# Kernel optimization log

Hardware: AMD Instinct MI355X
Metric: run time of the kernel (lower is better)

The kernel has to match this reference:

```python
import jax, jax.numpy as jnp
import numpy as np

FEAT_DIM = 4
TOKEN_DIM = 256
HIDDEN = [256, 256]
B, N, T = 512, 512, 4
BN_EPS = 1e-5


def setup_inputs() -> dict:
    key = jax.random.key(0)
    ks = jax.random.split(key, 10)
    bbox_ltwh = jax.random.uniform(ks[0], (B, N, T, FEAT_DIM), dtype=jnp.float32)
    mask = jax.random.randint(ks[1], (B, N), 0, 2).astype(bool)
    # MLP params: Linear(4->256)+BN+ReLU, Linear(256->256)+BN+ReLU, Linear(256->256)
    def lin(k, fan_in, fan_out):
        bound = 1.0 / np.sqrt(fan_in)
        kw, kb = jax.random.split(k)
        W = jax.random.uniform(kw, (fan_in, fan_out), minval=-bound, maxval=bound, dtype=jnp.float32)
        b = jax.random.uniform(kb, (fan_out,), minval=-bound, maxval=bound, dtype=jnp.float32)
        return W, b
    W1, b1 = lin(ks[2], FEAT_DIM, HIDDEN[0])
    W2, b2 = lin(ks[3], HIDDEN[0], HIDDEN[1])
    W3, b3 = lin(ks[4], HIDDEN[1], TOKEN_DIM)
    g1 = jnp.ones((HIDDEN[0],), jnp.float32); be1 = jnp.zeros((HIDDEN[0],), jnp.float32)
    g2 = jnp.ones((HIDDEN[1],), jnp.float32); be2 = jnp.zeros((HIDDEN[1],), jnp.float32)
    return {"bbox_ltwh": bbox_ltwh, "mask": mask,
            "W1": W1, "b1": b1, "g1": g1, "be1": be1,
            "W2": W2, "b2": b2, "g2": g2, "be2": be2,
            "W3": W3, "b3": b3}


def _masked_bn(h, m, cnt, gamma, beta):
    # BatchNorm1d (training mode) over only the valid (masked-in) rows.
    mu = jnp.sum(h * m, axis=0) / cnt
    var = jnp.sum(jnp.square(h - mu) * m, axis=0) / cnt
    return (h - mu) * jax.lax.rsqrt(var + BN_EPS) * gamma + beta


def reference(bbox_ltwh, mask, W1, b1, g1, be1, W2, b2, g2, be2, W3, b3):
    # last bbox of each tracklet: [B, N, 4] -> [B*N, 4]
    x = bbox_ltwh[:, :, 0].reshape(-1, FEAT_DIM)
    m = mask.reshape(-1).astype(x.dtype)[:, None]  # [B*N, 1]
    cnt = jnp.maximum(jnp.sum(m), 1.0)
    # Equivalent to gather(valid) -> MLP -> scatter into zeros: compute on all
    # rows with BN statistics taken over valid rows only, then zero invalid rows.
    h = jax.nn.relu(_masked_bn(x @ W1 + b1, m, cnt, g1, be1))
    h = jax.nn.relu(_masked_bn(h @ W2 + b2, m, cnt, g2, be2))
    h = h @ W3 + b3
    out = (h * m).reshape(B, N, TOKEN_DIM)
    return out
```

## Files before the change

### kernel.cpp

```cpp
#include <hip/hip_runtime.h>

typedef __attribute__((ext_vector_type(8))) short short8;
typedef __attribute__((ext_vector_type(4))) float f32x4;

#define M_ROWS (512*512)
#define NTILES (M_ROWS/64)
#define GRID_SETUP 512
#define GRID_STATS 512
#define GRID_MLP 256
#define ROWS_MLP (M_ROWS/GRID_MLP)
#define TILES_MLP (ROWS_MLP/64)
#define BN_EPS_F 1e-5f

#define WS_P1   64
#define WS_CNT  12352
#define WS_A1   12416
#define WS_D1   13440
#define WS_A2   13696
#define WS_C2   13952
#define WS_W2T  14336
#define WS_W3T  47104
#define WS_P2   79872

__device__ __forceinline__ float load_mask(const void* mp, int fmt, int row) {
  return fmt ? (((const unsigned char*)mp)[row] ? 1.f : 0.f)
             : (((const int*)mp)[row] ? 1.f : 0.f);
}

__device__ __forceinline__ ushort f2bf(float f) {
  unsigned int u = __float_as_uint(f);
  u += 0x7FFFu + ((u >> 16) & 1u);
  return (ushort)(u >> 16);
}

__device__ __forceinline__ void barrier_lds() {
  __builtin_amdgcn_sched_barrier(0);
  asm volatile("s_waitcnt lgkmcnt(0)");
  __builtin_amdgcn_sched_barrier(0);
  __builtin_amdgcn_s_barrier();
  __builtin_amdgcn_sched_barrier(0);
}

__device__ __forceinline__ void compute_h1(
    const float (*xs)[4], ushort* h1s, int t,
    const float a1c[4][2], const float d1c[2]) {
  const int c0 = (t & 127) * 2;
  const int r0 = (t >> 7) * 32;
  #pragma unroll 4
  for (int rr = 0; rr < 32; ++rr) {
    const int r = r0 + rr;
    const f32x4 xv = *(const f32x4*)&xs[r][0];
    float v0 = d1c[0], v1 = d1c[1];
    v0 = fmaf(xv.x, a1c[0][0], v0); v1 = fmaf(xv.x, a1c[0][1], v1);
    v0 = fmaf(xv.y, a1c[1][0], v0); v1 = fmaf(xv.y, a1c[1][1], v1);
    v0 = fmaf(xv.z, a1c[2][0], v0); v1 = fmaf(xv.z, a1c[2][1], v1);
    v0 = fmaf(xv.w, a1c[3][0], v0); v1 = fmaf(xv.w, a1c[3][1], v1);
    v0 = fmaxf(v0, 0.f); v1 = fmaxf(v1, 0.f);
    unsigned int pk = (unsigned int)f2bf(v0) | ((unsigned int)f2bf(v1) << 16);
    unsigned int byte = (unsigned int)r*512u + (unsigned int)c0*2u;
    byte ^= (unsigned int)(r & 7) << 4;
    *(unsigned int*)((char*)h1s + byte) = pk;
  }
}

__device__ __forceinline__ void load_aF(const ushort* h1s, int lane, int ks,
                                        int kb, short8 aF[4]) {
  #pragma unroll
  for (int rf = 0; rf < 4; ++rf) {
    const int row = rf*16 + (lane & 15);
    unsigned int byte = (unsigned int)row*512u + (unsigned int)((ks*32 + kb)*2);
    byte ^= (unsigned int)(row & 7) << 4;
    aF[rf] = *(const short8*)((const char*)h1s + byte);
  }
}

__device__ __forceinline__ void gemm_reg(const ushort* h1s,
    const short8 Br[4][8], int lane, f32x4 acc[4][4]) {
  const int kb = (lane >> 4) * 8;
  #pragma unroll
  for (int ks = 0; ks < 8; ++ks) {
    short8 aF[4];
    load_aF(h1s, lane, ks, kb, aF);
    #pragma unroll
    for (int cf = 0; cf < 4; ++cf)
      #pragma unroll
      for (int rf = 0; rf < 4; ++rf)
        acc[rf][cf] = __builtin_amdgcn_mfma_f32_16x16x32_bf16(
            aF[rf], Br[cf][ks], acc[rf][cf], 0, 0, 0);
  }
}

__device__ __forceinline__ void load_B(const ushort* __restrict__ Wt,
                                       int lane, int wave, short8 Br[4][8]) {
  const int kb = (lane >> 4) * 8;
  const ushort* wp = Wt + (size_t)(wave*64 + (lane & 15))*256 + kb;
  #pragma unroll
  for (int cf = 0; cf < 4; ++cf)
    #pragma unroll
    for (int ks = 0; ks < 8; ++ks)
      Br[cf][ks] = *(const short8*)(wp + cf*4096 + ks*32);
}

__global__ __launch_bounds__(256) void setup_kernel(
    const float* __restrict__ bbox, const void* __restrict__ maskp,
    const float* __restrict__ W2, const float* __restrict__ W3,
    float* __restrict__ wsf) {
  __shared__ int s_fmt;
  __shared__ float red[256][22];
  const int t = threadIdx.x, b = blockIdx.x;
  if (t == 0) s_fmt = 0;
  __syncthreads();
  {
    const uint4 v = ((const uint4*)maskp)[t];
    if (((v.x | v.y | v.z | v.w) & 0xFFFFFF00u) != 0u) s_fmt = 1;
  }
  __syncthreads();
  const int fmt = s_fmt;

  float own[21];
  #pragma unroll
  for (int i = 0; i < 21; ++i) own[i] = 0.f;
  #pragma unroll
  for (int i = 0; i < 2; ++i) {
    const int row = b*512 + i*256 + t;
    const float m = load_mask(maskp, fmt, row);
    if (m != 0.f) {
      float4 x4 = *(const float4*)(bbox + (size_t)row * 16);
      float xv[4] = {x4.x, x4.y, x4.z, x4.w};
      own[0] += 1.f;
      #pragma unroll
      for (int i2 = 0; i2 < 4; ++i2) {
        own[1+i2] += xv[i2];
        #pragma unroll
        for (int j = 0; j < 4; ++j)
          own[5+i2*4+j] = fmaf(xv[i2], xv[j], own[5+i2*4+j]);
      }
    }
  }
  #pragma unroll
  for (int s = 0; s < 21; ++s) red[t][s] = own[s];
  __syncthreads();
  for (int off = 128; off > 0; off >>= 1) {
    if (t < off) {
      #pragma unroll
      for (int s = 0; s < 21; ++s) red[t][s] += red[t+off][s];
    }
    __syncthreads();
  }
  if (t < 21) wsf[WS_P1 + b*24 + t] = red[0][t];

  if (b < 256) {
    ((ushort*)(wsf + WS_W2T))[t*256 + b] = f2bf(W2[b*256 + t]);
  } else {
    const int bb = b - 256;
    ((ushort*)(wsf + WS_W3T))[t*256 + bb] = f2bf(W3[bb*256 + t]);
  }
}

__global__ __launch_bounds__(256) void finalize1_kernel(
    const float* __restrict__ part, const float* __restrict__ W1,
    const float* __restrict__ b1, const float* __restrict__ g1,
    const float* __restrict__ be1, float* __restrict__ wsf) {
  __shared__ float red[256][22];
  __shared__ float sarr[21];
  const int t = threadIdx.x;
  #pragma unroll
  for (int s = 0; s < 21; ++s)
    red[t][s] = part[t*24 + s] + part[(t+256)*24 + s];
  __syncthreads();
  for (int off = 128; off > 0; off >>= 1) {
    if (t < off) {
      #pragma unroll
      for (int s = 0; s < 21; ++s) red[t][s] += red[t+off][s];
    }
    __syncthreads();
  }
  if (t < 21) sarr[t] = red[0][t];
  __syncthreads();
  float s[21];
  #pragma unroll
  for (int i = 0; i < 21; ++i) s[i] = sarr[i];
  const float cnt = fmaxf(s[0], 1.f);
  float w[4] = {W1[t], W1[256+t], W1[512+t], W1[768+t]};
  const float b1f = b1[t];
  float sw = 0.f;
  #pragma unroll
  for (int k = 0; k < 4; ++k) sw = fmaf(s[1+k], w[k], sw);
  float qf = 0.f;
  #pragma unroll
  for (int i = 0; i < 4; ++i)
    #pragma unroll
    for (int j = 0; j < 4; ++j) qf = fmaf(s[5+i*4+j]*w[i], w[j], qf);
  const float mu  = sw/cnt + b1f;
  const float eh2 = (qf + 2.f*b1f*sw)/cnt + b1f*b1f;
  const float var = fmaxf(eh2 - mu*mu, 0.f);
  const float a1  = g1[t] * rsqrtf(var + BN_EPS_F);
  const float c1  = be1[t] - mu*a1;
  #pragma unroll
  for (int k = 0; k < 4; ++k) wsf[WS_A1 + k*256 + t] = w[k]*a1;
  wsf[WS_D1 + t] = fmaf(b1f, a1, c1);
  if (t == 0) wsf[WS_CNT] = cnt;
}

__global__ __launch_bounds__(256, 2) void stats2_mfma(
    const float* __restrict__ bbox, const void* __restrict__ maskp,
    const float* wsf, const float* __restrict__ b2,
    float* __restrict__ part2) {
  __shared__ float xs[64][4];
  __shared__ float ms[64];
  __shared__ ushort h1s[64*256];
  __shared__ int s_fmt;
  const int t = threadIdx.x, lane = t & 63, wave = t >> 6;
  if (t == 0) s_fmt = 0;
  __syncthreads();
  {
    const uint4 v = ((const uint4*)maskp)[t];
    if (((v.x | v.y | v.z | v.w) & 0xFFFFFF00u) != 0u) s_fmt = 1;
  }
  __syncthreads();
  const int fmt = s_fmt;
  float a1c[4][2], d1c[2];
  {
    const int c0 = (t & 127) * 2;
    #pragma unroll
    for (int j = 0; j < 4; ++j) {
      a1c[j][0] = wsf[WS_A1 + j*256 + c0];
      a1c[j][1] = wsf[WS_A1 + j*256 + c0 + 1];
    }
    d1c[0] = wsf[WS_D1 + c0]; d1c[1] = wsf[WS_D1 + c0 + 1];
  }
  short8 B2r[4][8];
  load_B((const ushort*)(wsf + WS_W2T), lane, wave, B2r);
  float b2v[4];
  #pragma unroll
  for (int cf = 0; cf < 4; ++cf) b2v[cf] = b2[wave*64 + cf*16 + (lane & 15)];
  float pS[4] = {0,0,0,0}, pQ[4] = {0,0,0,0};

  for (int tile = blockIdx.x; tile < NTILES; tile += GRID_STATS) {
    const int row0 = tile << 6;
    __syncthreads();
    if (t < 64) {
      float4 x4 = *(const float4*)(bbox + (size_t)(row0 + t) * 16);
      xs[t][0] = x4.x; xs[t][1] = x4.y; xs[t][2] = x4.z; xs[t][3] = x4.w;
      ms[t] = load_mask(maskp, fmt, row0 + t);
    }
    __syncthreads();
    compute_h1(xs, h1s, t, a1c, d1c);
    __syncthreads();
    f32x4 acc[4][4];
    #pragma unroll
    for (int rf = 0; rf < 4; ++rf)
      #pragma unroll
      for (int cf = 0; cf < 4; ++cf)
        acc[rf][cf] = (f32x4){b2v[cf], b2v[cf], b2v[cf], b2v[cf]};
    gemm_reg(h1s, B2r, lane, acc);
    float mr[4][4];
    #pragma unroll
    for (int rf = 0; rf < 4; ++rf)
      #pragma unroll
      for (int r = 0; r < 4; ++r)
        mr[rf][r] = ms[rf*16 + ((lane >> 4) * 4) + r];
    #pragma unroll
    for (int cf = 0; cf < 4; ++cf)
      #pragma unroll
      for (int rf = 0; rf < 4; ++rf)
        #pragma unroll
        for (int r = 0; r < 4; ++r) {
          const float m = mr[rf][r];
          const float v = acc[rf][cf][r];
          pS[cf] = fmaf(m, v, pS[cf]);
          pQ[cf] = fmaf(m*v, v, pQ[cf]);
        }
  }
  #pragma unroll
  for (int cf = 0; cf < 4; ++cf) {
    pS[cf] += __shfl_xor(pS[cf], 16); pS[cf] += __shfl_xor(pS[cf], 32);
    pQ[cf] += __shfl_xor(pQ[cf], 16); pQ[cf] += __shfl_xor(pQ[cf], 32);
  }
  if (lane < 16) {
    #pragma unroll
    for (int cf = 0; cf < 4; ++cf) {
      const int col = wave*64 + cf*16 + lane;
      part2[(size_t)blockIdx.x*512 + col] = pS[cf];
      part2[(size_t)blockIdx.x*512 + 256 + col] = pQ[cf];
    }
  }
}

__global__ __launch_bounds__(256) void finalize2_kernel(
    float* __restrict__ wsf, const float* __restrict__ g2,
    const float* __restrict__ be2) {
  const int f = blockIdx.x, t = threadIdx.x;
  const float* part2 = wsf + WS_P2;
  float s1 = 0.f, s2 = 0.f;
  for (int b = t; b < GRID_STATS; b += 256) {
    s1 += part2[(size_t)b*512 + f];
    s2 += part2[(size_t)b*512 + 256 + f];
  }
  __shared__ float r1[256], r2[256];
  r1[t] = s1; r2[t] = s2;
  __syncthreads();
  for (int off = 128; off > 0; off >>= 1) {
    if (t < off) { r1[t] += r1[t+off]; r2[t] += r2[t+off]; }
    __syncthreads();
  }
  if (t == 0) {
    const float cnt = wsf[WS_CNT];
    const float mu  = r1[0]/cnt;
    const float var = fmaxf(r2[0]/cnt - mu*mu, 0.f);
    const float a2  = g2[f] * rsqrtf(var + BN_EPS_F);
    wsf[WS_A2 + f] = a2;
    wsf[WS_C2 + f] = be2[f] - mu*a2;
  }
}

__global__ __launch_bounds__(256, 1) void mlp3_mfma(
    const float* __restrict__ bbox, const void* __restrict__ maskp,
    const float* wsf, const float* __restrict__ b2,
    const float* __restrict__ b3, float* __restrict__ out) {
  __shared__ ushort h1s[64*256];
  __shared__ float xst[ROWS_MLP][4];
  __shared__ float mst[ROWS_MLP];
  __shared__ int s_fmt;
  const int t = threadIdx.x, lane = t & 63, wave = t >> 6;
  if (t == 0) s_fmt = 0;
  __syncthreads();
  {
    const uint4 v = ((const uint4*)maskp)[t];
    if (((v.x | v.y | v.z | v.w) & 0xFFFFFF00u) != 0u) s_fmt = 1;
  }
  __syncthreads();
  const int fmt = s_fmt;
  const int row_base = blockIdx.x * ROWS_MLP;

  #pragma unroll
  for (int i = 0; i < ROWS_MLP/256; ++i) {
    const int r = i*256 + t;
    float4 x4 = *(const float4*)(bbox + (size_t)(row_base + r) * 16);
    xst[r][0] = x4.x; xst[r][1] = x4.y; xst[r][2] = x4.z; xst[r][3] = x4.w;
    mst[r] = load_mask(maskp, fmt, row_base + r);
  }
  float a1c[4][2], d1c[2];
  {
    const int c0 = (t & 127) * 2;
    #pragma unroll
    for (int j = 0; j < 4; ++j) {
      a1c[j][0] = wsf[WS_A1 + j*256 + c0];
      a1c[j][1] = wsf[WS_A1 + j*256 + c0 + 1];
    }
    d1c[0] = wsf[WS_D1 + c0]; d1c[1] = wsf[WS_D1 + c0 + 1];
  }
  short8 B2r[4][8], B3r[4][8];
  load_B((const ushort*)(wsf + WS_W2T), lane, wave, B2r);
  load_B((const ushort*)(wsf + WS_W3T), lane, wave, B3r);
  float b2v[4], b3v[4], a2v[4], c2v[4];
  #pragma unroll
  for (int cf = 0; cf < 4; ++cf) {
    const int col = wave*64 + cf*16 + (lane & 15);
    b2v[cf] = b2[col]; b3v[cf] = b3[col];
    a2v[cf] = wsf[WS_A2 + col]; c2v[cf] = wsf[WS_C2 + col];
  }
  __syncthreads();

  for (int tile = 0; tile < TILES_MLP; ++tile) {
    const int r0 = tile * 64;
    compute_h1(&xst[r0], h1s, t, a1c, d1c);
    barrier_lds();
    f32x4 acc[4][4];
    #pragma unroll
    for (int rf = 0; rf < 4; ++rf)
      #pragma unroll
      for (int cf = 0; cf < 4; ++cf)
        acc[rf][cf] = (f32x4){b2v[cf], b2v[cf], b2v[cf], b2v[cf]};
    gemm_reg(h1s, B2r, lane, acc);
    barrier_lds();
    #pragma unroll
    for (int rf = 0; rf < 4; ++rf)
      #pragma unroll
      for (int cf = 0; cf < 4; ++cf) {
        const int col = wave*64 + cf*16 + (lane & 15);
        #pragma unroll
        for (int r = 0; r < 4; ++r) {
          const float v = fmaxf(fmaf(acc[rf][cf][r], a2v[cf], c2v[cf]), 0.f);
          const int row = rf*16 + ((lane >> 4) * 4) + r;
          unsigned int byte = (unsigned int)row*512u + (unsigned int)col*2u;
          byte ^= (unsigned int)(row & 7) << 4;
          *(ushort*)((char*)h1s + byte) = f2bf(v);
        }
      }
    barrier_lds();
    #pragma unroll
    for (int rf = 0; rf < 4; ++rf)
      #pragma unroll
      for (int cf = 0; cf < 4; ++cf)
        acc[rf][cf] = (f32x4){b3v[cf], b3v[cf], b3v[cf], b3v[cf]};
    gemm_reg(h1s, B3r, lane, acc);
    float mr[4][4];
    #pragma unroll
    for (int rf = 0; rf < 4; ++rf)
      #pragma unroll
      for (int r = 0; r < 4; ++r)
        mr[rf][r] = mst[r0 + rf*16 + ((lane >> 4) * 4) + r];
    #pragma unroll
    for (int rf = 0; rf < 4; ++rf)
      #pragma unroll
      for (int cf = 0; cf < 4; ++cf) {
        const int col = wave*64 + cf*16 + (lane & 15);
        #pragma unroll
        for (int r = 0; r < 4; ++r) {
          const int lrow = rf*16 + ((lane >> 4) * 4) + r;
          out[(size_t)(row_base + r0 + lrow)*256 + col] =
              acc[rf][cf][r] * mr[rf][r];
        }
      }
    barrier_lds();
  }
}

extern "C" void kernel_launch(void* const* d_in, const int* in_sizes, int n_in,
                              void* d_out, int out_size, void* d_ws, size_t ws_size,
                              hipStream_t stream) {
  (void)in_sizes; (void)n_in; (void)out_size; (void)ws_size;
  const float* bbox = (const float*)d_in[0];
  const void*  maskp= d_in[1];
  const float* W1 = (const float*)d_in[2];
  const float* b1 = (const float*)d_in[3];
  const float* g1 = (const float*)d_in[4];
  const float* be1= (const float*)d_in[5];
  const float* W2 = (const float*)d_in[6];
  const float* b2 = (const float*)d_in[7];
  const float* g2 = (const float*)d_in[8];
  const float* be2= (const float*)d_in[9];
  const float* W3 = (const float*)d_in[10];
  const float* b3 = (const float*)d_in[11];
  float* out = (float*)d_out;
  float* wsf = (float*)d_ws;

  hipLaunchKernelGGL(setup_kernel, dim3(GRID_SETUP), dim3(256), 0, stream,
                     bbox, maskp, W2, W3, wsf);
  hipLaunchKernelGGL(finalize1_kernel, dim3(1), dim3(256), 0, stream,
                     wsf + WS_P1, W1, b1, g1, be1, wsf);
  hipLaunchKernelGGL(stats2_mfma, dim3(GRID_STATS), dim3(256), 0, stream,
                     bbox, maskp, wsf, b2, wsf + WS_P2);
  hipLaunchKernelGGL(finalize2_kernel, dim3(256), dim3(256), 0, stream,
                     wsf, g2, be2);
  hipLaunchKernelGGL(mlp3_mfma, dim3(GRID_MLP), dim3(256), 0, stream,
                     bbox, maskp, wsf, b2, b3, out);
}
```

Baseline: 205.4 us.

## Double-buffer h1 tile and interleave next-tile layer-1 compute with GEMM2

```diff
diff --git a/kernel.cpp b/kernel.cpp
--- a/kernel.cpp
+++ b/kernel.cpp
@@ -63,6 +63,28 @@
   }
 }
 
+__device__ __forceinline__ void h1_chunk4(
+    const float (*xs)[4], ushort* h1s, int t,
+    const float a1c[4][2], const float d1c[2], int rbase) {
+  const int c0 = (t & 127) * 2;
+  const int r0 = (t >> 7) * 32 + rbase;
+  #pragma unroll
+  for (int rr = 0; rr < 4; ++rr) {
+    const int r = r0 + rr;
+    const f32x4 xv = *(const f32x4*)&xs[r][0];
+    float v0 = d1c[0], v1 = d1c[1];
+    v0 = fmaf(xv.x, a1c[0][0], v0); v1 = fmaf(xv.x, a1c[0][1], v1);
+    v0 = fmaf(xv.y, a1c[1][0], v0); v1 = fmaf(xv.y, a1c[1][1], v1);
+    v0 = fmaf(xv.z, a1c[2][0], v0); v1 = fmaf(xv.z, a1c[2][1], v1);
+    v0 = fmaf(xv.w, a1c[3][0], v0); v1 = fmaf(xv.w, a1c[3][1], v1);
+    v0 = fmaxf(v0, 0.f); v1 = fmaxf(v1, 0.f);
+    unsigned int pk = (unsigned int)f2bf(v0) | ((unsigned int)f2bf(v1) << 16);
+    unsigned int byte = (unsigned int)r*512u + (unsigned int)c0*2u;
+    byte ^= (unsigned int)(r & 7) << 4;
+    *(unsigned int*)((char*)h1s + byte) = pk;
+  }
+}
+
 __device__ __forceinline__ void load_aF(const ushort* h1s, int lane, int ks,
                                         int kb, short8 aF[4]) {
   #pragma unroll
@@ -318,7 +340,7 @@
     const float* __restrict__ bbox, const void* __restrict__ maskp,
     const float* wsf, const float* __restrict__ b2,
     const float* __restrict__ b3, float* __restrict__ out) {
-  __shared__ ushort h1s[64*256];
+  __shared__ ushort h1d[2][64*256];
   __shared__ float xst[ROWS_MLP][4];
   __shared__ float mst[ROWS_MLP];
   __shared__ int s_fmt;
@@ -361,18 +383,32 @@
     a2v[cf] = wsf[WS_A2 + col]; c2v[cf] = wsf[WS_C2 + col];
   }
   __syncthreads();
-
+  compute_h1(&xst[0], h1d[0], t, a1c, d1c);
+  barrier_lds();
+
+  const int kb = (lane >> 4) * 8;
   for (int tile = 0; tile < TILES_MLP; ++tile) {
-    const int r0 = tile * 64;
-    compute_h1(&xst[r0], h1s, t, a1c, d1c);
-    barrier_lds();
+    const int cur = tile & 1, nxt = cur ^ 1;
+    const bool hasNext = (tile + 1 < TILES_MLP);
+    const float (*xn)[4] = &xst[hasNext ? (tile+1)*64 : 0];
     f32x4 acc[4][4];
     #pragma unroll
     for (int rf = 0; rf < 4; ++rf)
       #pragma unroll
       for (int cf = 0; cf < 4; ++cf)
         acc[rf][cf] = (f32x4){b2v[cf], b2v[cf], b2v[cf], b2v[cf]};
-    gemm_reg(h1s, B2r, lane, acc);
+    #pragma unroll
+    for (int ks = 0; ks < 8; ++ks) {
+      if (hasNext) h1_chunk4(xn, h1d[nxt], t, a1c, d1c, ks*4);
+      short8 aF[4];
+      load_aF(h1d[cur], lane, ks, kb, aF);
+      #pragma unroll
+      for (int cf = 0; cf < 4; ++cf)
+        #pragma unroll
+        for (int rf = 0; rf < 4; ++rf)
+          acc[rf][cf] = __builtin_amdgcn_mfma_f32_16x16x32_bf16(
+              aF[rf], B2r[cf][ks], acc[rf][cf], 0, 0, 0);
+    }
     barrier_lds();
     #pragma unroll
     for (int rf = 0; rf < 4; ++rf)
@@ -385,7 +421,7 @@
           const int row = rf*16 + ((lane >> 4) * 4) + r;
           unsigned int byte = (unsigned int)row*512u + (unsigned int)col*2u;
           byte ^= (unsigned int)(row & 7) << 4;
-          *(ushort*)((char*)h1s + byte) = f2bf(v);
+          *(ushort*)((char*)h1d[cur] + byte) = f2bf(v);
         }
       }
     barrier_lds();
@@ -394,7 +430,8 @@
       #pragma unroll
       for (int cf = 0; cf < 4; ++cf)
         acc[rf][cf] = (f32x4){b3v[cf], b3v[cf], b3v[cf], b3v[cf]};
-    gemm_reg(h1s, B3r, lane, acc);
+    gemm_reg(h1d[cur], B3r, lane, acc);
+    const int r0 = tile * 64;
     float mr[4][4];
     #pragma unroll
     for (int rf = 0; rf < 4; ++rf)
```

Result: slower. 330.0 us (+60.7%).

## Warp-specialize MLP kernel into layer-2 producer and layer-3 consumer waves

Applied to the files above, without the earlier changes.

```diff
diff --git a/kernel.cpp b/kernel.cpp
--- a/kernel.cpp
+++ b/kernel.cpp
@@ -91,9 +91,9 @@
 }
 
 __device__ __forceinline__ void load_B(const ushort* __restrict__ Wt,
-                                       int lane, int wave, short8 Br[4][8]) {
+                                       int lane, int cwave, short8 Br[4][8]) {
   const int kb = (lane >> 4) * 8;
-  const ushort* wp = Wt + (size_t)(wave*64 + (lane & 15))*256 + kb;
+  const ushort* wp = Wt + (size_t)(cwave*64 + (lane & 15))*256 + kb;
   #pragma unroll
   for (int cf = 0; cf < 4; ++cf)
     #pragma unroll
@@ -314,18 +314,19 @@
   }
 }
 
-__global__ __launch_bounds__(256, 1) void mlp3_mfma(
+__global__ __launch_bounds__(512, 2) void mlp3_ws(
     const float* __restrict__ bbox, const void* __restrict__ maskp,
     const float* wsf, const float* __restrict__ b2,
     const float* __restrict__ b3, float* __restrict__ out) {
-  __shared__ ushort h1s[64*256];
+  __shared__ ushort h1buf[64*256];
+  __shared__ ushort h2buf[2][64*256];
   __shared__ float xst[ROWS_MLP][4];
   __shared__ float mst[ROWS_MLP];
   __shared__ int s_fmt;
   const int t = threadIdx.x, lane = t & 63, wave = t >> 6;
   if (t == 0) s_fmt = 0;
   __syncthreads();
-  {
+  if (t < 256) {
     const uint4 v = ((const uint4*)maskp)[t];
     if (((v.x | v.y | v.z | v.w) & 0xFFFFFF00u) != 0u) s_fmt = 1;
   }
@@ -334,86 +335,119 @@
   const int row_base = blockIdx.x * ROWS_MLP;
 
   #pragma unroll
-  for (int i = 0; i < ROWS_MLP/256; ++i) {
-    const int r = i*256 + t;
+  for (int i = 0; i < ROWS_MLP/512; ++i) {
+    const int r = i*512 + t;
     float4 x4 = *(const float4*)(bbox + (size_t)(row_base + r) * 16);
     xst[r][0] = x4.x; xst[r][1] = x4.y; xst[r][2] = x4.z; xst[r][3] = x4.w;
     mst[r] = load_mask(maskp, fmt, row_base + r);
   }
-  float a1c[4][2], d1c[2];
-  {
-    const int c0 = (t & 127) * 2;
-    #pragma unroll
-    for (int j = 0; j < 4; ++j) {
-      a1c[j][0] = wsf[WS_A1 + j*256 + c0];
-      a1c[j][1] = wsf[WS_A1 + j*256 + c0 + 1];
-    }
-    d1c[0] = wsf[WS_D1 + c0]; d1c[1] = wsf[WS_D1 + c0 + 1];
-  }
-  short8 B2r[4][8], B3r[4][8];
-  load_B((const ushort*)(wsf + WS_W2T), lane, wave, B2r);
-  load_B((const ushort*)(wsf + WS_W3T), lane, wave, B3r);
-  float b2v[4], b3v[4], a2v[4], c2v[4];
-  #pragma unroll
-  for (int cf = 0; cf < 4; ++cf) {
-    const int col = wave*64 + cf*16 + (lane & 15);
-    b2v[cf] = b2[col]; b3v[cf] = b3[col];
-    a2v[cf] = wsf[WS_A2 + col]; c2v[cf] = wsf[WS_C2 + col];
-  }
-  __syncthreads();
-
-  for (int tile = 0; tile < TILES_MLP; ++tile) {
-    const int r0 = tile * 64;
-    compute_h1(&xst[r0], h1s, t, a1c, d1c);
-    barrier_lds();
-    f32x4 acc[4][4];
-    #pragma unroll
-    for (int rf = 0; rf < 4; ++rf)
-      #pragma unroll
-      for (int cf = 0; cf < 4; ++cf)
-        acc[rf][cf] = (f32x4){b2v[cf], b2v[cf], b2v[cf], b2v[cf]};
-    gemm_reg(h1s, B2r, lane, acc);
-    barrier_lds();
-    #pragma unroll
-    for (int rf = 0; rf < 4; ++rf)
-      #pragma unroll
-      for (int cf = 0; cf < 4; ++cf) {
-        const int col = wave*64 + cf*16 + (lane & 15);
-        #pragma unroll
-        for (int r = 0; r < 4; ++r) {
-          const float v = fmaxf(fmaf(acc[rf][cf][r], a2v[cf], c2v[cf]), 0.f);
-          const int row = rf*16 + ((lane >> 4) * 4) + r;
-          unsigned int byte = (unsigned int)row*512u + (unsigned int)col*2u;
-          byte ^= (unsigned int)(row & 7) << 4;
-          *(ushort*)((char*)h1s + byte) = f2bf(v);
+  __syncthreads();
+
+  if (wave < 4) {
+    float a1c[4][2], d1c[2];
+    {
+      const int c0 = (t & 127) * 2;
+      #pragma unroll
+      for (int j = 0; j < 4; ++j) {
+        a1c[j][0] = wsf[WS_A1 + j*256 + c0];
+        a1c[j][1] = wsf[WS_A1 + j*256 + c0 + 1];
+      }
+      d1c[0] = wsf[WS_D1 + c0]; d1c[1] = wsf[WS_D1 + c0 + 1];
+    }
+    short8 B2r[4][8];
+    load_B((const ushort*)(wsf + WS_W2T), lane, wave, B2r);
+    float b2v[4], a2v[4], c2v[4];
+    #pragma unroll
+    for (int cf = 0; cf < 4; ++cf) {
+      const int col = wave*64 + cf*16 + (lane & 15);
+      b2v[cf] = b2[col];
+      a2v[cf] = wsf[WS_A2 + col]; c2v[cf] = wsf[WS_C2 + col];
+    }
+    for (int tile = 0; tile < TILES_MLP; ++tile) {
+      compute_h1(&xst[tile*64], h1buf, t, a1c, d1c);
+      barrier_lds();
+      f32x4 acc[4][4];
+      #pragma unroll
+      for (int rf = 0; rf < 4; ++rf)
+        #pragma unroll
+        for (int cf = 0; cf < 4; ++cf)
+          acc[rf][cf] = (f32x4){b2v[cf], b2v[cf], b2v[cf], b2v[cf]};
+      gemm_reg(h1buf, B2r, lane, acc);
+      ushort* h2 = h2buf[tile & 1];
+      #pragma unroll
+      for (int rf = 0; rf < 4; ++rf)
+        #pragma unroll
+        for (int cf = 0; cf < 4; ++cf) {
+          const int col = wave*64 + cf*16 + (lane & 15);
+          #pragma unroll
+          for (int r = 0; r < 4; ++r) {
+            const float v = fmaxf(fmaf(acc[rf][cf][r], a2v[cf], c2v[cf]), 0.f);
+            const int row = rf*16 + ((lane >> 4) * 4) + r;
+            unsigned int byte = (unsigned int)row*512u + (unsigned int)col*2u;
+            byte ^= (unsigned int)(row & 7) << 4;
+            *(ushort*)((char*)h2 + byte) = f2bf(v);
+          }
         }
+      barrier_lds();
+    }
+  } else {
+    const int cwave = wave - 4;
+    short8 B3r[4][8];
+    load_B((const ushort*)(wsf + WS_W3T), lane, cwave, B3r);
+    float b3v[4];
+    #pragma unroll
+    for (int cf = 0; cf < 4; ++cf) b3v[cf] = b3[cwave*64 + cf*16 + (lane & 15)];
+
+    for (int tile = 0; tile < TILES_MLP; ++tile) {
+      if (tile > 0) {
+        const int pt = tile - 1;
+        f32x4 acc[4][4];
+        #pragma unroll
+        for (int rf = 0; rf < 4; ++rf)
+          #pragma unroll
+          for (int cf = 0; cf < 4; ++cf)
+            acc[rf][cf] = (f32x4){b3v[cf], b3v[cf], b3v[cf], b3v[cf]};
+        gemm_reg(h2buf[pt & 1], B3r, lane, acc);
+        const int r0 = pt * 64;
+        #pragma unroll
+        for (int rf = 0; rf < 4; ++rf)
+          #pragma unroll
+          for (int cf = 0; cf < 4; ++cf) {
+            const int col = cwave*64 + cf*16 + (lane & 15);
+            #pragma unroll
+            for (int r = 0; r < 4; ++r) {
+              const int lrow = rf*16 + ((lane >> 4) * 4) + r;
+              out[(size_t)(row_base + r0 + lrow)*256 + col] =
+                  acc[rf][cf][r] * mst[r0 + lrow];
+            }
+          }
       }
-    barrier_lds();
-    #pragma unroll
-    for (int rf = 0; rf < 4; ++rf)
-      #pragma unroll
-      for (int cf = 0; cf < 4; ++cf)
-        acc[rf][cf] = (f32x4){b3v[cf], b3v[cf], b3v[cf], b3v[cf]};
-    gemm_reg(h1s, B3r, lane, acc);
-    float mr[4][4];
-    #pragma unroll
-    for (int rf = 0; rf < 4; ++rf)
-      #pragma unroll
-      for (int r = 0; r < 4; ++r)
-        mr[rf][r] = mst[r0 + rf*16 + ((lane >> 4) * 4) + r];
-    #pragma unroll
-    for (int rf = 0; rf < 4; ++rf)
-      #pragma unroll
-      for (int cf = 0; cf < 4; ++cf) {
-        const int col = wave*64 + cf*16 + (lane & 15);
-        #pragma unroll
-        for (int r = 0; r < 4; ++r) {
-          const int lrow = rf*16 + ((lane >> 4) * 4) + r;
-          out[(size_t)(row_base + r0 + lrow)*256 + col] =
-              acc[rf][cf][r] * mr[rf][r];
+      barrier_lds();
+      barrier_lds();
+    }
+    {
+      const int pt = TILES_MLP - 1;
+      f32x4 acc[4][4];
+      #pragma unroll
+      for (int rf = 0; rf < 4; ++rf)
+        #pragma unroll
+        for (int cf = 0; cf < 4; ++cf)
+          acc[rf][cf] = (f32x4){b3v[cf], b3v[cf], b3v[cf], b3v[cf]};
+      gemm_reg(h2buf[pt & 1], B3r, lane, acc);
+      const int r0 = pt * 64;
+      #pragma unroll
+      for (int rf = 0; rf < 4; ++rf)
+        #pragma unroll
+        for (int cf = 0; cf < 4; ++cf) {
+          const int col = cwave*64 + cf*16 + (lane & 15);
+          #pragma unroll
+          for (int r = 0; r < 4; ++r) {
+            const int lrow = rf*16 + ((lane >> 4) * 4) + r;
+            out[(size_t)(row_base + r0 + lrow)*256 + col] =
+                acc[rf][cf][r] * mst[r0 + lrow];
+          }
         }
-      }
-    barrier_lds();
+    }
   }
 }
 
@@ -444,6 +478,6 @@
                      bbox, maskp, wsf, b2, wsf + WS_P2);
   hipLaunchKernelGGL(finalize2_kernel, dim3(256), dim3(256), 0, stream,
                      wsf, g2, be2);
-  hipLaunchKernelGGL(mlp3_mfma, dim3(GRID_MLP), dim3(256), 0, stream,
+  hipLaunchKernelGGL(mlp3_ws, dim3(GRID_MLP), dim3(512), 0, stream,
                      bbox, maskp, wsf, b2, b3, out);
 }
```

Measured after the change: 558.8 us. 172% more time.
